# Kernel optimization log

Hardware: AMD Instinct MI355X
Metric: run time of the kernel (lower is better)

The kernel has to match this reference:

```python
import jax, jax.numpy as jnp
import numpy as np

N_NODES = 1_000_000
N_EDGES = 16_000_000
N_GRAPHS = 1024


def setup_inputs() -> dict:
    key = jax.random.key(0)
    ks = jax.random.split(key, 8)
    features = jax.random.normal(ks[0], (N_NODES, 10), dtype=jnp.float32)
    src = jax.random.randint(ks[1], (N_EDGES,), 0, N_NODES, dtype=jnp.int32)
    dst = jax.random.randint(ks[2], (N_EDGES,), 0, N_NODES, dtype=jnp.int32)
    graph_ids = jnp.sort(jax.random.randint(ks[3], (N_NODES,), 0, N_GRAPHS, dtype=jnp.int32))
    W1 = jax.random.normal(ks[4], (10, 8), dtype=jnp.float32) * (1.0 / np.sqrt(10))
    b1 = jnp.zeros((8,), dtype=jnp.float32)
    W2 = jax.random.normal(ks[5], (8, 4), dtype=jnp.float32) * (1.0 / np.sqrt(8))
    b2 = jnp.zeros((4,), dtype=jnp.float32)
    Wo = jax.random.normal(ks[6], (4, 1), dtype=jnp.float32) * 0.5
    bo = jnp.zeros((1,), dtype=jnp.float32)
    return {"features": features, "src": src, "dst": dst, "graph_ids": graph_ids,
            "W1": W1, "b1": b1, "W2": W2, "b2": b2, "Wo": Wo, "bo": bo}


def _graph_conv(x, W, b, src, dst, out_norm, in_norm):
    # DGL GraphConv, norm='both': h = D_in^{-1/2} A (D_out^{-1/2} x) W + b
    x = x * out_norm[:, None]
    x = x @ W  # project first (in_feats >= out_feats) to shrink messages
    agg = jax.ops.segment_sum(x[src], dst, num_segments=N_NODES)
    return agg * in_norm[:, None] + b


def reference(features, src, dst, graph_ids, W1, b1, W2, b2, Wo, bo):
    ones_e = jnp.ones((src.shape[0],), dtype=jnp.float32)
    out_deg = jax.ops.segment_sum(ones_e, src, num_segments=N_NODES)
    in_deg = jax.ops.segment_sum(ones_e, dst, num_segments=N_NODES)
    out_norm = jnp.clip(out_deg, 1.0, None) ** -0.5
    in_norm = jnp.clip(in_deg, 1.0, None) ** -0.5

    h = jax.nn.relu(_graph_conv(features, W1, b1, src, dst, out_norm, in_norm))
    h = jax.nn.relu(_graph_conv(h, W2, b2, src, dst, out_norm, in_norm))

    # dgl.mean_nodes: per-graph mean of node features
    gsum = jax.ops.segment_sum(h, graph_ids, num_segments=N_GRAPHS)
    gcnt = jax.ops.segment_sum(jnp.ones((N_NODES,), dtype=jnp.float32), graph_ids,
                               num_segments=N_GRAPHS)
    gmean = gsum / jnp.clip(gcnt, 1.0, None)[:, None]

    return jax.nn.sigmoid(gmean @ Wo + bo).reshape(-1)
```

## Files before the change

kernel.cpp:

```cpp
#include <hip/hip_runtime.h>
#include <hip/hip_fp16.h>
#include <math.h>


#define BSHIFT 10
#define BMASK  1023u
#define NBKT   1024
#define CAP    17408u
#define SRT    ((CAP + 511) / 512)
#define NBIN   2048
#define HSTAGE (CAP / 2)

#define PTH2   1024
#define EPT2   16
#define CHUNK2 (PTH2 * EPT2)

typedef float v2f __attribute__((ext_vector_type(2)));
typedef unsigned int u32x4 __attribute__((ext_vector_type(4)));
typedef unsigned int u32x2 __attribute__((ext_vector_type(2)));

template <bool HI>
__device__ inline v2f up8(unsigned int w) {
    return __builtin_amdgcn_cvt_pk_f32_fp8((int)w, HI);
}
__device__ inline unsigned int pk4(float a, float b, float c, float d) {
    int r = __builtin_amdgcn_cvt_pk_fp8_f32(a, b, 0, false);
    r = __builtin_amdgcn_cvt_pk_fp8_f32(c, d, r, true);
    return (unsigned int)r;
}
__device__ inline unsigned int pkh(float a, float b) {
    __half2 h = __floats2half2_rn(a, b);
    union { __half2 h; unsigned int u; } c; c.h = h; return c.u;
}
__device__ inline v2f uph(unsigned int u) {
    union { unsigned int u; __half2 h; } c; c.u = u;
    float2 f = __half22float2(c.h);
    v2f r; r.x = f.x; r.y = f.y; return r;
}
__device__ inline void acc8(float* acc, uint2 v) {
    v2f f0 = up8<false>(v.x);
    v2f f1 = up8<true>(v.x);
    v2f f2 = up8<false>(v.y);
    v2f f3 = up8<true>(v.y);
    acc[0] += f0.x; acc[1] += f0.y; acc[2] += f1.x; acc[3] += f1.y;
    acc[4] += f2.x; acc[5] += f2.y; acc[6] += f3.x; acc[7] += f3.y;
}
__device__ inline void acc4(float* acc, unsigned int q) {
    v2f f0 = up8<false>(q);
    v2f f1 = up8<true>(q);
    acc[0] += f0.x; acc[1] += f0.y; acc[2] += f1.x; acc[3] += f1.y;
}

__global__ __launch_bounds__(PTH2) void k_part_src(const int* __restrict__ src,
                                                   unsigned short* __restrict__ ps,
                                                   unsigned int* __restrict__ cur,
                                                   int n_edges) {
    __shared__ unsigned int hist[NBKT];
    __shared__ unsigned int scanA[NBKT];
    __shared__ unsigned int scanB[NBKT];
    __shared__ unsigned int gbase[NBKT];
    __shared__ unsigned short stage[CHUNK2];
    const int tid = threadIdx.x;
    const int e0 = blockIdx.x * CHUNK2;
    hist[tid] = 0;
    __syncthreads();
    unsigned int sv[EPT2];
    unsigned int rk[EPT2];
#pragma unroll
    for (int k = 0; k < EPT2; ++k) {
        int e = e0 + k * PTH2 + tid;
        sv[k] = 0xFFFFFFFFu;
        if (e < n_edges) {
            unsigned int s = (unsigned int)src[e];
            sv[k] = s;
            rk[k] = atomicAdd(&hist[s >> BSHIFT], 1u);
        }
    }
    __syncthreads();
    const unsigned int cnt = hist[tid];
    scanA[tid] = cnt;
    __syncthreads();
    unsigned int* pin = scanA;
    unsigned int* pout = scanB;
    for (int off = 1; off < NBKT; off <<= 1) {
        unsigned int v = pin[tid];
        if (tid >= off) v += pin[tid - off];
        pout[tid] = v;
        __syncthreads();
        unsigned int* t = pin; pin = pout; pout = t;
    }
    gbase[tid] = atomicAdd(&cur[tid], cnt);
    __syncthreads();
#pragma unroll
    for (int k = 0; k < EPT2; ++k) {
        if (sv[k] != 0xFFFFFFFFu) {
            unsigned int b = sv[k] >> BSHIFT;
            unsigned int start = (b == 0) ? 0u : pin[b - 1];
            stage[start + rk[k]] = (unsigned short)(sv[k] & BMASK);
        }
    }
    __syncthreads();
    const int wid = tid >> 6, lane = tid & 63;
    for (int b = wid; b < NBKT; b += (PTH2 >> 6)) {
        unsigned int start = (b == 0) ? 0u : pin[b - 1];
        unsigned int cb = pin[b] - start;
        unsigned int gb = gbase[b];
        for (unsigned int o = lane; o < cb; o += 64)
            ps[(size_t)b * CAP + gb + o] = stage[start + o];
    }
}

__global__ __launch_bounds__(512) void k_deg_src(const unsigned short* __restrict__ ps,
                                                 const unsigned int* __restrict__ cur,
                                                 float* __restrict__ onorm, int n_nodes) {
    __shared__ unsigned int cnt[1 << BSHIFT];
    const int b = blockIdx.x, tid = threadIdx.x;
    for (int i = tid; i < (1 << BSHIFT); i += 512) cnt[i] = 0;
    __syncthreads();
    const unsigned int n = cur[b];
    const unsigned int base = (unsigned int)b * CAP;
    const unsigned int nfull = n & ~4095u;
    for (unsigned int i0 = 0; i0 < nfull; i0 += 4096) {
        uint4 p = *(const uint4*)(ps + base + i0 + (unsigned int)tid * 8u);
        unsigned int w[4] = {p.x, p.y, p.z, p.w};
#pragma unroll
        for (int k = 0; k < 4; ++k) {
            atomicAdd(&cnt[w[k] & 0xFFFFu], 1u);
            atomicAdd(&cnt[w[k] >> 16], 1u);
        }
    }
    for (unsigned int i = nfull + tid; i < n; i += 512) atomicAdd(&cnt[ps[base + i]], 1u);
    __syncthreads();
    for (int r = tid; r < (1 << BSHIFT); r += 512) {
        int node = (b << BSHIFT) + r;
        if (node < n_nodes) onorm[node] = rsqrtf(fmaxf((float)cnt[r], 1.0f));
    }
}

__global__ __launch_bounds__(PTH2) void k_part_dst(const int* __restrict__ src,
                                                   const int* __restrict__ dst,
                                                   unsigned int* __restrict__ pd,
                                                   unsigned int* __restrict__ cur,
                                                   int n_edges) {
    __shared__ unsigned int hist[NBKT];
    __shared__ unsigned int scanA[NBKT];
    __shared__ unsigned int scanB[NBKT];
    __shared__ unsigned int gbase[NBKT];
    __shared__ unsigned int stage[CHUNK2];
    const int tid = threadIdx.x;
    const int e0 = blockIdx.x * CHUNK2;
    hist[tid] = 0;
    __syncthreads();
    unsigned int wv[EPT2];
    unsigned int bb[EPT2];
    unsigned int rk[EPT2];
#pragma unroll
    for (int k = 0; k < EPT2; ++k) {
        int e = e0 + k * PTH2 + tid;
        bb[k] = 0xFFFFFFFFu;
        if (e < n_edges) {
            unsigned int d = (unsigned int)dst[e];
            unsigned int s = (unsigned int)src[e];
            unsigned int b = d >> BSHIFT;
            wv[k] = (s << BSHIFT) | (d & BMASK);
            bb[k] = b;
            rk[k] = atomicAdd(&hist[b], 1u);
        }
    }
    __syncthreads();
    const unsigned int cnt = hist[tid];
    scanA[tid] = cnt;
    __syncthreads();
    unsigned int* pin = scanA;
    unsigned int* pout = scanB;
    for (int off = 1; off < NBKT; off <<= 1) {
        unsigned int v = pin[tid];
        if (tid >= off) v += pin[tid - off];
        pout[tid] = v;
        __syncthreads();
        unsigned int* t = pin; pin = pout; pout = t;
    }
    gbase[tid] = atomicAdd(&cur[tid], cnt);
    __syncthreads();
#pragma unroll
    for (int k = 0; k < EPT2; ++k) {
        if (bb[k] != 0xFFFFFFFFu) {
            unsigned int start = (bb[k] == 0) ? 0u : pin[bb[k] - 1];
            stage[start + rk[k]] = wv[k];
        }
    }
    __syncthreads();
    const int wid = tid >> 6, lane = tid & 63;
    for (int b = wid; b < NBKT; b += (PTH2 >> 6)) {
        unsigned int start = (b == 0) ? 0u : pin[b - 1];
        unsigned int cb = pin[b] - start;
        unsigned int gb = gbase[b];
        for (unsigned int o = lane; o < cb; o += 64)
            pd[(size_t)b * CAP + gb + o] = stage[start + o];
    }
}

__global__ __launch_bounds__(512) void k_sort_dst(unsigned int* __restrict__ pd,
                                                  const unsigned int* __restrict__ cur,
                                                  unsigned int* __restrict__ starts) {
    __shared__ unsigned int sA[NBIN];
    __shared__ unsigned int sB[NBIN];
    __shared__ unsigned int curs[NBIN];
    __shared__ unsigned int stage[HSTAGE];
    const int b = blockIdx.x, tid = threadIdx.x;
    for (int i = tid; i < NBIN; i += 512) sA[i] = 0;
    __syncthreads();
    const unsigned int n = cur[b];
    const unsigned int base = (unsigned int)b * CAP;
    unsigned int rv[SRT];
#pragma unroll
    for (int k = 0; k < SRT; ++k) {
        unsigned int i = (unsigned int)k * 512u + (unsigned int)tid;
        rv[k] = 0xFFFFFFFFu;
        if (i < n) {
            rv[k] = pd[base + i];
            unsigned int key = ((rv[k] & BMASK) << 1) | ((rv[k] >> 29) & 1u);
            atomicAdd(&sA[key], 1u);
        }
    }
    __syncthreads();
    unsigned int* pin = sA;
    unsigned int* pout = sB;
    for (int off = 1; off < NBIN; off <<= 1) {
        for (int r = tid; r < NBIN; r += 512) {
            unsigned int v = pin[r];
            if (r >= off) v += pin[r - off];
            pout[r] = v;
        }
        __syncthreads();
        unsigned int* t = pin; pin = pout; pout = t;
    }
    for (int r = tid; r < NBIN; r += 512) {
        unsigned int st = (r == 0) ? 0u : pin[r - 1];
        curs[r] = st;
        starts[(size_t)b * NBIN + r] = st;
    }
    __syncthreads();
    unsigned int pos[SRT];
#pragma unroll
    for (int k = 0; k < SRT; ++k) {
        pos[k] = 0xFFFFFFFFu;
        if (rv[k] != 0xFFFFFFFFu) {
            unsigned int key = ((rv[k] & BMASK) << 1) | ((rv[k] >> 29) & 1u);
            pos[k] = atomicAdd(&curs[key], 1u);
        }
    }
    __syncthreads();
#pragma unroll
    for (int k = 0; k < SRT; ++k)
        if (pos[k] < HSTAGE) stage[pos[k]] = rv[k];
    __syncthreads();
    const unsigned int lim0 = (n < HSTAGE) ? n : HSTAGE;
    for (unsigned int i = tid; i < lim0; i += 512) pd[base + i] = stage[i];
    __syncthreads();
#pragma unroll
    for (int k = 0; k < SRT; ++k)
        if (pos[k] != 0xFFFFFFFFu && pos[k] >= HSTAGE) stage[pos[k] - HSTAGE] = rv[k];
    __syncthreads();
    for (unsigned int i = HSTAGE + tid; i < n; i += 512) pd[base + i] = stage[i - HSTAGE];
}

__global__ void k_node1(const float* __restrict__ feat, const float* __restrict__ W1,
                        const float* __restrict__ onorm, uint2* __restrict__ y1,
                        int n_nodes) {
    int i = blockIdx.x * blockDim.x + threadIdx.x;
    if (i >= n_nodes) return;
    float on = onorm[i];
    const float* fr = feat + (size_t)i * 10;
    float f[10];
#pragma unroll
    for (int k = 0; k < 10; ++k) f[k] = fr[k];
    float acc[8];
#pragma unroll
    for (int j = 0; j < 8; ++j) acc[j] = 0.0f;
#pragma unroll
    for (int k = 0; k < 10; ++k)
#pragma unroll
        for (int j = 0; j < 8; ++j) acc[j] = fmaf(f[k], W1[k * 8 + j], acc[j]);
    uint2 o;
    o.x = pk4(acc[0] * on, acc[1] * on, acc[2] * on, acc[3] * on);
    o.y = pk4(acc[4] * on, acc[5] * on, acc[6] * on, acc[7] * on);
    y1[i] = o;
}

__global__ __launch_bounds__(1024) void k_agg1a(const unsigned int* __restrict__ pd,
                                                const unsigned int* __restrict__ starts,
                                                const uint2* __restrict__ y,
                                                u32x4* __restrict__ part, int n_nodes) {
    const int b = blockIdx.x;
    const int r = threadIdx.x;
    const int node = (b << BSHIFT) + r;
    if (node >= n_nodes) return;
    const unsigned int base = (unsigned int)b * CAP;
    const unsigned int* st = starts + ((size_t)b << 11);
    unsigned int s = st[2 * r];
    unsigned int e = st[2 * r + 1];
    float acc[8];
#pragma unroll
    for (int j = 0; j < 8; ++j) acc[j] = 0.0f;
    unsigned int i = s;
    for (; i + 4 <= e; i += 4) {
        unsigned int w0 = pd[base + i + 0];
        unsigned int w1 = pd[base + i + 1];
        unsigned int w2 = pd[base + i + 2];
        unsigned int w3 = pd[base + i + 3];
        uint2 v0 = y[w0 >> BSHIFT];
        uint2 v1 = y[w1 >> BSHIFT];
        uint2 v2 = y[w2 >> BSHIFT];
        uint2 v3 = y[w3 >> BSHIFT];
        acc8(acc, v0); acc8(acc, v1); acc8(acc, v2); acc8(acc, v3);
    }
    for (; i < e; ++i) acc8(acc, y[pd[base + i] >> BSHIFT]);
    u32x4 p;
    p.x = pkh(acc[0], acc[1]);
    p.y = pkh(acc[2], acc[3]);
    p.z = pkh(acc[4], acc[5]);
    p.w = pkh(acc[6], acc[7]);
    __builtin_nontemporal_store(p, part + node);
}

__global__ __launch_bounds__(1024) void k_agg1b(const unsigned int* __restrict__ pd,
                                                const unsigned int* __restrict__ cur,
                                                const unsigned int* __restrict__ starts,
                                                const uint2* __restrict__ y,
                                                const u32x4* __restrict__ part,
                                                const float* __restrict__ b1,
                                                const float* __restrict__ W2,
                                                const float* __restrict__ onorm,
                                                unsigned int* __restrict__ y2, int n_nodes) {
    const int b = blockIdx.x;
    const int r = threadIdx.x;
    const int node = (b << BSHIFT) + r;
    if (node >= n_nodes) return;
    const unsigned int base = (unsigned int)b * CAP;
    const unsigned int* st = starts + ((size_t)b << 11);
    unsigned int s0 = st[2 * r];
    unsigned int s = st[2 * r + 1];
    unsigned int e = (r == 1023) ? cur[b] : st[2 * r + 2];
    float acc[8];
#pragma unroll
    for (int j = 0; j < 8; ++j) acc[j] = 0.0f;
    unsigned int i = s;
    for (; i + 4 <= e; i += 4) {
        unsigned int w0 = pd[base + i + 0];
        unsigned int w1 = pd[base + i + 1];
        unsigned int w2 = pd[base + i + 2];
        unsigned int w3 = pd[base + i + 3];
        uint2 v0 = y[w0 >> BSHIFT];
        uint2 v1 = y[w1 >> BSHIFT];
        uint2 v2 = y[w2 >> BSHIFT];
        uint2 v3 = y[w3 >> BSHIFT];
        acc8(acc, v0); acc8(acc, v1); acc8(acc, v2); acc8(acc, v3);
    }
    for (; i < e; ++i) acc8(acc, y[pd[base + i] >> BSHIFT]);
    u32x4 p = __builtin_nontemporal_load(part + node);
    v2f q0 = uph(p.x), q1 = uph(p.y), q2 = uph(p.z), q3 = uph(p.w);
    acc[0] += q0.x; acc[1] += q0.y; acc[2] += q1.x; acc[3] += q1.y;
    acc[4] += q2.x; acc[5] += q2.y; acc[6] += q3.x; acc[7] += q3.y;
    float inn = rsqrtf(fmaxf((float)(e - s0), 1.0f));
    float h[8];
#pragma unroll
    for (int j = 0; j < 8; ++j) h[j] = fmaxf(fmaf(acc[j], inn, b1[j]), 0.0f);
    float z[4] = {0.0f, 0.0f, 0.0f, 0.0f};
#pragma unroll
    for (int k = 0; k < 8; ++k)
#pragma unroll
        for (int j = 0; j < 4; ++j) z[j] = fmaf(h[k], W2[k * 4 + j], z[j]);
    float on = onorm[node];
    y2[node] = pk4(z[0] * on, z[1] * on, z[2] * on, z[3] * on);
}

__global__ __launch_bounds__(1024) void k_agg2a(const unsigned int* __restrict__ pd,
                                                const unsigned int* __restrict__ starts,
                                                const unsigned int* __restrict__ y,
                                                u32x2* __restrict__ part, int n_nodes) {
    const int b = blockIdx.x;
    const int r = threadIdx.x;
    const int node = (b << BSHIFT) + r;
    if (node >= n_nodes) return;
    const unsigned int base = (unsigned int)b * CAP;
    const unsigned int* st = starts + ((size_t)b << 11);
    unsigned int s = st[2 * r];
    unsigned int e = st[2 * r + 1];
    float acc[4] = {0.0f, 0.0f, 0.0f, 0.0f};
    unsigned int i = s;
    for (; i + 4 <= e; i += 4) {
        unsigned int w0 = pd[base + i + 0];
        unsigned int w1 = pd[base + i + 1];
        unsigned int w2 = pd[base + i + 2];
        unsigned int w3 = pd[base + i + 3];
        unsigned int q0 = y[w0 >> BSHIFT];
        unsigned int q1 = y[w1 >> BSHIFT];
        unsigned int q2 = y[w2 >> BSHIFT];
        unsigned int q3 = y[w3 >> BSHIFT];
        acc4(acc, q0); acc4(acc, q1); acc4(acc, q2); acc4(acc, q3);
    }
    for (; i < e; ++i) acc4(acc, y[pd[base + i] >> BSHIFT]);
    u32x2 p;
    p.x = pkh(acc[0], acc[1]);
    p.y = pkh(acc[2], acc[3]);
    __builtin_nontemporal_store(p, part + node);
}

__global__ __launch_bounds__(1024) void k_agg2b(const unsigned int* __restrict__ pd,
                                                const unsigned int* __restrict__ cur,
                                                const unsigned int* __restrict__ starts,
                                                const unsigned int* __restrict__ y,
                                                const u32x2* __restrict__ part,
                                                const float* __restrict__ b2,
                                                const int* __restrict__ gid,
                                                float* __restrict__ gsum,
                                                float* __restrict__ gcnt, int n_nodes) {
    const int b = blockIdx.x;
    const int r = threadIdx.x;
    const int node = (b << BSHIFT) + r;
    const int lane = threadIdx.x & 63;
    int g = -1;
    float v0 = 0.f, v1 = 0.f, v2 = 0.f, v3 = 0.f, c = 0.f;
    if (node < n_nodes) {
        const unsigned int base = (unsigned int)b * CAP;
        const unsigned int* st = starts + ((size_t)b << 11);
        unsigned int s0 = st[2 * r];
        unsigned int s = st[2 * r + 1];
        unsigned int e = (r == 1023) ? cur[b] : st[2 * r + 2];
        float acc[4] = {0.0f, 0.0f, 0.0f, 0.0f};
        unsigned int i = s;
        for (; i + 4 <= e; i += 4) {
            unsigned int w0 = pd[base + i + 0];
            unsigned int w1 = pd[base + i + 1];
            unsigned int w2 = pd[base + i + 2];
            unsigned int w3 = pd[base + i + 3];
            unsigned int q0 = y[w0 >> BSHIFT];
            unsigned int q1 = y[w1 >> BSHIFT];
            unsigned int q2 = y[w2 >> BSHIFT];
            unsigned int q3 = y[w3 >> BSHIFT];
            acc4(acc, q0); acc4(acc, q1); acc4(acc, q2); acc4(acc, q3);
        }
        for (; i < e; ++i) acc4(acc, y[pd[base + i] >> BSHIFT]);
        u32x2 p = __builtin_nontemporal_load(part + node);
        v2f p0 = uph(p.x), p1 = uph(p.y);
        acc[0] += p0.x; acc[1] += p0.y; acc[2] += p1.x; acc[3] += p1.y;
        float inn = rsqrtf(fmaxf((float)(e - s0), 1.0f));
        v0 = fmaxf(fmaf(acc[0], inn, b2[0]), 0.0f);
        v1 = fmaxf(fmaf(acc[1], inn, b2[1]), 0.0f);
        v2 = fmaxf(fmaf(acc[2], inn, b2[2]), 0.0f);
        v3 = fmaxf(fmaf(acc[3], inn, b2[3]), 0.0f);
        c = 1.0f;
        g = gid[node];
    }
#pragma unroll
    for (int sft = 1; sft < 64; sft <<= 1) {
        int go   = __shfl_down(g, sft);
        float t0 = __shfl_down(v0, sft);
        float t1 = __shfl_down(v1, sft);
        float t2 = __shfl_down(v2, sft);
        float t3 = __shfl_down(v3, sft);
        float tc = __shfl_down(c, sft);
        if (lane + sft < 64 && go == g) {
            v0 += t0; v1 += t1; v2 += t2; v3 += t3; c += tc;
        }
    }
    int gp = __shfl_up(g, 1);
    bool head = (lane == 0) || (gp != g);
    if (g >= 0 && head) {
        unsafeAtomicAdd(&gsum[g * 4 + 0], v0);
        unsafeAtomicAdd(&gsum[g * 4 + 1], v1);
        unsafeAtomicAdd(&gsum[g * 4 + 2], v2);
        unsafeAtomicAdd(&gsum[g * 4 + 3], v3);
        unsafeAtomicAdd(&gcnt[g], c);
    }
}

__global__ void k_final(const float* __restrict__ gsum, const float* __restrict__ gcnt,
                        const float* __restrict__ Wo, const float* __restrict__ bo,
                        float* __restrict__ out, int n_graphs) {
    int i = blockIdx.x * blockDim.x + threadIdx.x;
    if (i >= n_graphs) return;
    float inv = 1.0f / fmaxf(gcnt[i], 1.0f);
    float z = bo[0];
#pragma unroll
    for (int j = 0; j < 4; ++j) z = fmaf(gsum[i * 4 + j] * inv, Wo[j], z);
    out[i] = 1.0f / (1.0f + expf(-z));
}

extern "C" void kernel_launch(void* const* d_in, const int* in_sizes, int n_in,
                              void* d_out, int out_size, void* d_ws, size_t ws_size,
                              hipStream_t stream) {
    const float* feat = (const float*)d_in[0];
    const int*   src  = (const int*)d_in[1];
    const int*   dst  = (const int*)d_in[2];
    const int*   gid  = (const int*)d_in[3];
    const float* W1   = (const float*)d_in[4];
    const float* b1   = (const float*)d_in[5];
    const float* W2   = (const float*)d_in[6];
    const float* b2   = (const float*)d_in[7];
    const float* Wo   = (const float*)d_in[8];
    const float* bo   = (const float*)d_in[9];
    float* out = (float*)d_out;

    const int n_nodes  = in_sizes[0] / 10;
    const int n_edges  = in_sizes[1];
    const int n_graphs = out_size;
    const int nbk_used = (n_nodes + (1 << BSHIFT) - 1) >> BSHIFT;

    unsigned int* ws32 = (unsigned int*)d_ws;
    const size_t PDW = (size_t)NBKT * CAP;
    const size_t n = (size_t)n_nodes;
    unsigned int*   pd     = ws32;
    unsigned short* ps     = (unsigned short*)ws32;
    unsigned int*   cs     = ws32 + PDW;
    unsigned int*   cd     = cs + NBKT;
    float*          gsum   = (float*)(cd + NBKT);
    float*          gcnt   = gsum + 4 * (size_t)n_graphs;
    float*          onorm  = gcnt + n_graphs;
    unsigned int*   starts = (unsigned int*)(onorm + n);
    unsigned int*   y1     = starts + (size_t)NBKT * NBIN;
    unsigned int*   y2     = y1 + 2 * n;
    u32x4*          part4  = (u32x4*)(y2 + n);
    u32x2*          part2  = (u32x2*)part4;

    (void)hipMemsetAsync(cs, 0, (2 * NBKT + 5 * (size_t)n_graphs) * sizeof(unsigned int),
                         stream);

    const int nchunk2 = (n_edges + CHUNK2 - 1) / CHUNK2;
    const int B = 256;

    k_part_src<<<nchunk2, PTH2, 0, stream>>>(src, ps, cs, n_edges);
    k_deg_src<<<nbk_used, 512, 0, stream>>>(ps, cs, onorm, n_nodes);
    k_part_dst<<<nchunk2, PTH2, 0, stream>>>(src, dst, pd, cd, n_edges);
    k_sort_dst<<<nbk_used, 512, 0, stream>>>(pd, cd, starts);
    k_node1<<<(n_nodes + B - 1) / B, B, 0, stream>>>(feat, W1, onorm, (uint2*)y1, n_nodes);
    k_agg1a<<<nbk_used, 1024, 0, stream>>>(pd, starts, (const uint2*)y1, part4, n_nodes);
    k_agg1b<<<nbk_used, 1024, 0, stream>>>(pd, cd, starts, (const uint2*)y1, part4, b1,
                                           W2, onorm, y2, n_nodes);
    k_agg2a<<<nbk_used, 1024, 0, stream>>>(pd, starts, y2, part2, n_nodes);
    k_agg2b<<<nbk_used, 1024, 0, stream>>>(pd, cd, starts, y2, part2, b2, gid, gsum,
                                           gcnt, n_nodes);
    k_final<<<(n_graphs + B - 1) / B, B, 0, stream>>>(gsum, gcnt, Wo, bo, out, n_graphs);
}
```

Baseline: 640.4 us.

## Fuse src/dst edge partitioning into one kernel with wave-shuffle scans

Merges the separate source and destination bucket-partition kernels into one kernel. It now loads edges as int4 vectors, and each thread handles four contiguous edges per group. The LDS Hillis-Steele prefix scans in the partition and sort kernels become wave-shuffle scans, which cuts barriers and LDS traffic. The ushort src-partition buffer moves to the later workspace region so it can coexist with the dst partition; this relies on that region not yet being in use when the partition kernel runs.

```diff
diff --git a/kernel.cpp b/kernel.cpp
--- a/kernel.cpp
+++ b/kernel.cpp
@@ -14,6 +14,7 @@
 #define PTH2   1024
 #define EPT2   16
 #define CHUNK2 (PTH2 * EPT2)
+#define NW2    (PTH2 / 64)
 
 typedef float v2f __attribute__((ext_vector_type(2)));
 typedef unsigned int u32x4 __attribute__((ext_vector_type(4)));
@@ -51,62 +52,160 @@
     acc[0] += f0.x; acc[1] += f0.y; acc[2] += f1.x; acc[3] += f1.y;
 }
 
-__global__ __launch_bounds__(PTH2) void k_part_src(const int* __restrict__ src,
-                                                   unsigned short* __restrict__ ps,
-                                                   unsigned int* __restrict__ cur,
-                                                   int n_edges) {
-    __shared__ unsigned int hist[NBKT];
-    __shared__ unsigned int scanA[NBKT];
-    __shared__ unsigned int scanB[NBKT];
-    __shared__ unsigned int gbase[NBKT];
-    __shared__ unsigned short stage[CHUNK2];
+__device__ inline unsigned int scan1024(unsigned int v, unsigned int* wsum, int tid) {
+    const int lane = tid & 63, wid = tid >> 6;
+    unsigned int x = v;
+#pragma unroll
+    for (int o = 1; o < 64; o <<= 1) {
+        unsigned int t = __shfl_up(x, o);
+        if (lane >= o) x += t;
+    }
+    if (lane == 63) wsum[wid] = x;
+    __syncthreads();
+    if (wid == 0) {
+        unsigned int y = (lane < NW2) ? wsum[lane] : 0u;
+#pragma unroll
+        for (int o = 1; o < NW2; o <<= 1) {
+            unsigned int t = __shfl_up(y, o);
+            if (lane >= o) y += t;
+        }
+        if (lane < NW2) wsum[lane] = y;
+    }
+    __syncthreads();
+    return x + (wid ? wsum[wid - 1] : 0u);
+}
+
+__global__ __launch_bounds__(PTH2, 8) void k_part(const int* __restrict__ src,
+                                                  const int* __restrict__ dst,
+                                                  unsigned short* __restrict__ ps,
+                                                  unsigned int* __restrict__ pd,
+                                                  unsigned int* __restrict__ cs,
+                                                  unsigned int* __restrict__ cd,
+                                                  int n_edges) {
+    __shared__ unsigned int pin[NBKT];
+    __shared__ unsigned int gaddr[NBKT];
+    __shared__ unsigned int wsum[NW2];
+    __shared__ unsigned int stageD[CHUNK2];
+    unsigned short* stageS = (unsigned short*)stageD;
     const int tid = threadIdx.x;
+    const int lane = tid & 63, wid = tid >> 6;
     const int e0 = blockIdx.x * CHUNK2;
-    hist[tid] = 0;
+
+    pin[tid] = 0;
     __syncthreads();
     unsigned int sv[EPT2];
-    unsigned int rk[EPT2];
-#pragma unroll
-    for (int k = 0; k < EPT2; ++k) {
-        int e = e0 + k * PTH2 + tid;
-        sv[k] = 0xFFFFFFFFu;
-        if (e < n_edges) {
-            unsigned int s = (unsigned int)src[e];
-            sv[k] = s;
-            rk[k] = atomicAdd(&hist[s >> BSHIFT], 1u);
-        }
-    }
-    __syncthreads();
-    const unsigned int cnt = hist[tid];
-    scanA[tid] = cnt;
-    __syncthreads();
-    unsigned int* pin = scanA;
-    unsigned int* pout = scanB;
-    for (int off = 1; off < NBKT; off <<= 1) {
-        unsigned int v = pin[tid];
-        if (tid >= off) v += pin[tid - off];
-        pout[tid] = v;
-        __syncthreads();
-        unsigned int* t = pin; pin = pout; pout = t;
-    }
-    gbase[tid] = atomicAdd(&cur[tid], cnt);
+    unsigned int rks[EPT2];
+#pragma unroll
+    for (int k4 = 0; k4 < EPT2 / 4; ++k4) {
+        int e = e0 + (k4 * PTH2 + tid) * 4;
+        if (e + 3 < n_edges) {
+            int4 s4 = *(const int4*)(src + e);
+            sv[k4 * 4 + 0] = (unsigned int)s4.x;
+            sv[k4 * 4 + 1] = (unsigned int)s4.y;
+            sv[k4 * 4 + 2] = (unsigned int)s4.z;
+            sv[k4 * 4 + 3] = (unsigned int)s4.w;
+        } else {
+#pragma unroll
+            for (int j = 0; j < 4; ++j)
+                sv[k4 * 4 + j] = (e + j < n_edges) ? (unsigned int)src[e + j]
+                                                   : 0xFFFFFFFFu;
+        }
+    }
+#pragma unroll
+    for (int k = 0; k < EPT2; ++k)
+        if (sv[k] != 0xFFFFFFFFu) rks[k] = atomicAdd(&pin[sv[k] >> BSHIFT], 1u);
+    __syncthreads();
+    {
+        unsigned int cnt = pin[tid];
+        unsigned int incl = scan1024(cnt, wsum, tid);
+        unsigned int gb = atomicAdd(&cs[tid], cnt);
+        pin[tid] = incl;
+        gaddr[tid] = gb - (incl - cnt);
+    }
     __syncthreads();
 #pragma unroll
     for (int k = 0; k < EPT2; ++k) {
         if (sv[k] != 0xFFFFFFFFu) {
             unsigned int b = sv[k] >> BSHIFT;
             unsigned int start = (b == 0) ? 0u : pin[b - 1];
-            stage[start + rk[k]] = (unsigned short)(sv[k] & BMASK);
-        }
-    }
-    __syncthreads();
-    const int wid = tid >> 6, lane = tid & 63;
-    for (int b = wid; b < NBKT; b += (PTH2 >> 6)) {
+            stageS[start + rks[k]] = (unsigned short)(sv[k] & BMASK);
+        }
+    }
+    __syncthreads();
+    for (int b = wid; b < NBKT; b += NW2) {
         unsigned int start = (b == 0) ? 0u : pin[b - 1];
-        unsigned int cb = pin[b] - start;
-        unsigned int gb = gbase[b];
-        for (unsigned int o = lane; o < cb; o += 64)
-            ps[(size_t)b * CAP + gb + o] = stage[start + o];
+        unsigned int end = pin[b];
+        unsigned int ga = gaddr[b];
+        for (unsigned int i = start + lane; i < end; i += 64) {
+            unsigned int off = ga + i;
+            ps[(size_t)b * CAP + off] = stageS[i];
+        }
+    }
+    __syncthreads();
+
+    pin[tid] = 0;
+    __syncthreads();
+    unsigned int wv[EPT2];
+    unsigned int rkd[EPT2];
+#pragma unroll
+    for (int k4 = 0; k4 < EPT2 / 4; ++k4) {
+        int e = e0 + (k4 * PTH2 + tid) * 4;
+        if (e + 3 < n_edges) {
+            int4 d4 = *(const int4*)(dst + e);
+            int4 s4 = *(const int4*)(src + e);
+            unsigned int dd[4] = {(unsigned int)d4.x, (unsigned int)d4.y,
+                                  (unsigned int)d4.z, (unsigned int)d4.w};
+            unsigned int ss[4] = {(unsigned int)s4.x, (unsigned int)s4.y,
+                                  (unsigned int)s4.z, (unsigned int)s4.w};
+#pragma unroll
+            for (int j = 0; j < 4; ++j) {
+                unsigned int b = dd[j] >> BSHIFT;
+                wv[k4 * 4 + j] = (ss[j] << BSHIFT) | (dd[j] & BMASK);
+                unsigned int r = atomicAdd(&pin[b], 1u);
+                rkd[k4 * 4 + j] = (b << 20) | r;
+            }
+        } else {
+#pragma unroll
+            for (int j = 0; j < 4; ++j) {
+                if (e + j < n_edges) {
+                    unsigned int d = (unsigned int)dst[e + j];
+                    unsigned int s = (unsigned int)src[e + j];
+                    unsigned int b = d >> BSHIFT;
+                    wv[k4 * 4 + j] = (s << BSHIFT) | (d & BMASK);
+                    unsigned int r = atomicAdd(&pin[b], 1u);
+                    rkd[k4 * 4 + j] = (b << 20) | r;
+                } else {
+                    rkd[k4 * 4 + j] = 0xFFFFFFFFu;
+                }
+            }
+        }
+    }
+    __syncthreads();
+    {
+        unsigned int cnt = pin[tid];
+        unsigned int incl = scan1024(cnt, wsum, tid);
+        unsigned int gb = atomicAdd(&cd[tid], cnt);
+        pin[tid] = incl;
+        gaddr[tid] = gb - (incl - cnt);
+    }
+    __syncthreads();
+#pragma unroll
+    for (int k = 0; k < EPT2; ++k) {
+        if (rkd[k] != 0xFFFFFFFFu) {
+            unsigned int b = rkd[k] >> 20;
+            unsigned int start = (b == 0) ? 0u : pin[b - 1];
+            stageD[start + (rkd[k] & 0xFFFFFu)] = wv[k];
+        }
+    }
+    __syncthreads();
+    for (int b = wid; b < NBKT; b += NW2) {
+        unsigned int start = (b == 0) ? 0u : pin[b - 1];
+        unsigned int end = pin[b];
+        unsigned int ga = gaddr[b];
+        for (unsigned int i = start + lane; i < end; i += 64) {
+            unsigned int off = ga + i;
+            pd[(size_t)b * CAP + off] = stageD[i];
+        }
     }
 }
 
@@ -137,78 +236,16 @@
     }
 }
 
-__global__ __launch_bounds__(PTH2) void k_part_dst(const int* __restrict__ src,
-                                                   const int* __restrict__ dst,
-                                                   unsigned int* __restrict__ pd,
-                                                   unsigned int* __restrict__ cur,
-                                                   int n_edges) {
-    __shared__ unsigned int hist[NBKT];
-    __shared__ unsigned int scanA[NBKT];
-    __shared__ unsigned int scanB[NBKT];
-    __shared__ unsigned int gbase[NBKT];
-    __shared__ unsigned int stage[CHUNK2];
-    const int tid = threadIdx.x;
-    const int e0 = blockIdx.x * CHUNK2;
-    hist[tid] = 0;
-    __syncthreads();
-    unsigned int wv[EPT2];
-    unsigned int bb[EPT2];
-    unsigned int rk[EPT2];
-#pragma unroll
-    for (int k = 0; k < EPT2; ++k) {
-        int e = e0 + k * PTH2 + tid;
-        bb[k] = 0xFFFFFFFFu;
-        if (e < n_edges) {
-            unsigned int d = (unsigned int)dst[e];
-            unsigned int s = (unsigned int)src[e];
-            unsigned int b = d >> BSHIFT;
-            wv[k] = (s << BSHIFT) | (d & BMASK);
-            bb[k] = b;
-            rk[k] = atomicAdd(&hist[b], 1u);
-        }
-    }
-    __syncthreads();
-    const unsigned int cnt = hist[tid];
-    scanA[tid] = cnt;
-    __syncthreads();
-    unsigned int* pin = scanA;
-    unsigned int* pout = scanB;
-    for (int off = 1; off < NBKT; off <<= 1) {
-        unsigned int v = pin[tid];
-        if (tid >= off) v += pin[tid - off];
-        pout[tid] = v;
-        __syncthreads();
-        unsigned int* t = pin; pin = pout; pout = t;
-    }
-    gbase[tid] = atomicAdd(&cur[tid], cnt);
-    __syncthreads();
-#pragma unroll
-    for (int k = 0; k < EPT2; ++k) {
-        if (bb[k] != 0xFFFFFFFFu) {
-            unsigned int start = (bb[k] == 0) ? 0u : pin[bb[k] - 1];
-            stage[start + rk[k]] = wv[k];
-        }
-    }
-    __syncthreads();
-    const int wid = tid >> 6, lane = tid & 63;
-    for (int b = wid; b < NBKT; b += (PTH2 >> 6)) {
-        unsigned int start = (b == 0) ? 0u : pin[b - 1];
-        unsigned int cb = pin[b] - start;
-        unsigned int gb = gbase[b];
-        for (unsigned int o = lane; o < cb; o += 64)
-            pd[(size_t)b * CAP + gb + o] = stage[start + o];
-    }
-}
-
 __global__ __launch_bounds__(512) void k_sort_dst(unsigned int* __restrict__ pd,
                                                   const unsigned int* __restrict__ cur,
                                                   unsigned int* __restrict__ starts) {
-    __shared__ unsigned int sA[NBIN];
-    __shared__ unsigned int sB[NBIN];
+    __shared__ unsigned int pin[NBIN];
     __shared__ unsigned int curs[NBIN];
+    __shared__ unsigned int wsum[8];
     __shared__ unsigned int stage[HSTAGE];
     const int b = blockIdx.x, tid = threadIdx.x;
-    for (int i = tid; i < NBIN; i += 512) sA[i] = 0;
+    const int lane = tid & 63, wid = tid >> 6;
+    for (int i = tid; i < NBIN; i += 512) pin[i] = 0;
     __syncthreads();
     const unsigned int n = cur[b];
     const unsigned int base = (unsigned int)b * CAP;
@@ -220,25 +257,40 @@
         if (i < n) {
             rv[k] = pd[base + i];
             unsigned int key = ((rv[k] & BMASK) << 1) | ((rv[k] >> 29) & 1u);
-            atomicAdd(&sA[key], 1u);
-        }
-    }
-    __syncthreads();
-    unsigned int* pin = sA;
-    unsigned int* pout = sB;
-    for (int off = 1; off < NBIN; off <<= 1) {
-        for (int r = tid; r < NBIN; r += 512) {
-            unsigned int v = pin[r];
-            if (r >= off) v += pin[r - off];
-            pout[r] = v;
-        }
+            atomicAdd(&pin[key], 1u);
+        }
+    }
+    __syncthreads();
+    {
+        unsigned int a0 = pin[4 * tid + 0], a1 = pin[4 * tid + 1];
+        unsigned int a2 = pin[4 * tid + 2], a3 = pin[4 * tid + 3];
+        unsigned int ts = a0 + a1 + a2 + a3;
+        unsigned int x = ts;
+#pragma unroll
+        for (int o = 1; o < 64; o <<= 1) {
+            unsigned int t = __shfl_up(x, o);
+            if (lane >= o) x += t;
+        }
+        if (lane == 63) wsum[wid] = x;
         __syncthreads();
-        unsigned int* t = pin; pin = pout; pout = t;
-    }
-    for (int r = tid; r < NBIN; r += 512) {
-        unsigned int st = (r == 0) ? 0u : pin[r - 1];
-        curs[r] = st;
-        starts[(size_t)b * NBIN + r] = st;
+        if (wid == 0) {
+            unsigned int y = (lane < 8) ? wsum[lane] : 0u;
+#pragma unroll
+            for (int o = 1; o < 8; o <<= 1) {
+                unsigned int t = __shfl_up(y, o);
+                if (lane >= o) y += t;
+            }
+            if (lane < 8) wsum[lane] = y;
+        }
+        __syncthreads();
+        unsigned int ex = x - ts + (wid ? wsum[wid - 1] : 0u);
+        unsigned int i0 = ex + a0, i1 = i0 + a1, i2 = i1 + a2, i3 = i2 + a3;
+        pin[4 * tid + 0] = i0; pin[4 * tid + 1] = i1;
+        pin[4 * tid + 2] = i2; pin[4 * tid + 3] = i3;
+        curs[4 * tid + 0] = ex; curs[4 * tid + 1] = i0;
+        curs[4 * tid + 2] = i1; curs[4 * tid + 3] = i2;
+        unsigned int* sp = starts + ((size_t)b << 11) + 4 * tid;
+        sp[0] = ex; sp[1] = i0; sp[2] = i1; sp[3] = i2;
     }
     __syncthreads();
     unsigned int pos[SRT];
@@ -512,13 +564,13 @@
     const size_t PDW = (size_t)NBKT * CAP;
     const size_t n = (size_t)n_nodes;
     unsigned int*   pd     = ws32;
-    unsigned short* ps     = (unsigned short*)ws32;
     unsigned int*   cs     = ws32 + PDW;
     unsigned int*   cd     = cs + NBKT;
     float*          gsum   = (float*)(cd + NBKT);
     float*          gcnt   = gsum + 4 * (size_t)n_graphs;
     float*          onorm  = gcnt + n_graphs;
     unsigned int*   starts = (unsigned int*)(onorm + n);
+    unsigned short* ps     = (unsigned short*)starts;
     unsigned int*   y1     = starts + (size_t)NBKT * NBIN;
     unsigned int*   y2     = y1 + 2 * n;
     u32x4*          part4  = (u32x4*)(y2 + n);
@@ -530,9 +582,8 @@
     const int nchunk2 = (n_edges + CHUNK2 - 1) / CHUNK2;
     const int B = 256;
 
-    k_part_src<<<nchunk2, PTH2, 0, stream>>>(src, ps, cs, n_edges);
+    k_part<<<nchunk2, PTH2, 0, stream>>>(src, dst, ps, pd, cs, cd, n_edges);
     k_deg_src<<<nbk_used, 512, 0, stream>>>(ps, cs, onorm, n_nodes);
-    k_part_dst<<<nchunk2, PTH2, 0, stream>>>(src, dst, pd, cd, n_edges);
     k_sort_dst<<<nbk_used, 512, 0, stream>>>(pd, cd, starts);
     k_node1<<<(n_nodes + B - 1) / B, B, 0, stream>>>(feat, W1, onorm, (uint2*)y1, n_nodes);
     k_agg1a<<<nbk_used, 1024, 0, stream>>>(pd, starts, (const uint2*)y1, part4, n_nodes);
```

New measurement: 600.5 us. 1.07x faster.
